# Kernel tuning notes

Measured on AMD Instinct MI355X. Metric: run time of the kernel, lower is better.

The kernel has to match this reference:

```python
import jax, jax.numpy as jnp
import numpy as np

QUERY_DIM = 192
KEY_DIM = 64
DIM_OUT = 128
C = QUERY_DIM + KEY_DIM  # 256
N = 10000
E = 320000
M = 5000


def setup_inputs() -> dict:
    key = jax.random.key(0)
    ks = jax.random.split(key, 16)
    s = 1.0 / np.sqrt(C)
    inp = {
        "query": jax.random.normal(ks[0], (N, QUERY_DIM), jnp.float32),
        "key_idx": jax.random.randint(ks[1], (N,), 0, KEY_DIM),
        "edge_index": jax.random.randint(ks[2], (2, E), 0, N),
        "mask_idx": jnp.sort(jax.random.randint(ks[3], (M,), 0, N)),
        "Wq": jax.random.normal(ks[4], (C, C), jnp.float32) * s,
        "bq": jnp.zeros((C,), jnp.float32),
        "Wk": jax.random.normal(ks[5], (C, C), jnp.float32) * s,
        "bk": jnp.zeros((C,), jnp.float32),
        "Wv": jax.random.normal(ks[6], (C, C), jnp.float32) * s,
        "bv": jnp.zeros((C,), jnp.float32),
        "Ws": jax.random.normal(ks[7], (C, C), jnp.float32) * s,
        "bs": jnp.zeros((C,), jnp.float32),
        "Wo": jax.random.normal(ks[8], (KEY_DIM, DIM_OUT), jnp.float32) * (1.0 / np.sqrt(KEY_DIM)),
        "bo": jnp.zeros((DIM_OUT,), jnp.float32),
    }
    return inp


def reference(query, key_idx, edge_index, mask_idx, Wq, bq, Wk, bk, Wv, bv, Ws, bs, Wo, bo):
    # node features: [N, C] = concat(query, one_hot(key))
    x = jnp.concatenate([query, jax.nn.one_hot(key_idx, KEY_DIM, dtype=query.dtype)], axis=1)
    src, dst = edge_index[0], edge_index[1]  # messages flow src -> dst
    # node-level projections (dense GEMMs), then edge gather
    q_n = x @ Wq + bq
    k_n = x @ Wk + bk
    v_n = x @ Wv + bv
    q = q_n[dst]  # [E, C]
    k = k_n[src]
    v = v_n[src]
    score = jnp.sum(q * k, axis=-1) / jnp.sqrt(jnp.asarray(C, x.dtype))  # [E]
    # per-destination softmax over incoming edges
    m = jax.ops.segment_max(score, dst, num_segments=N)  # [N]
    m = jnp.where(jnp.isfinite(m), m, 0.0)
    e = jnp.exp(score - m[dst])
    denom = jax.ops.segment_sum(e, dst, num_segments=N)
    alpha = e / (denom[dst] + 1e-16)
    # scatter-aggregate weighted values + root/skip connection
    agg = jax.ops.segment_sum(alpha[:, None] * v, dst, num_segments=N)  # [N, C]
    out = agg + (x @ Ws + bs)
    h = jax.nn.relu(out[mask_idx])  # [M, C]
    h = h[:, QUERY_DIM:]  # [M, KEY_DIM]
    return h @ Wo + bo  # [M, DIM_OUT]
```

## Files before the change

kernel.cpp:

```cpp
#include <hip/hip_runtime.h>

#define QDIM 192
#define KDIM 64
#define CDIM 256
#define NCOLS 640
#define DOUT 128
#define CAP 128
#define NEG_INF __int_as_float(0xFF800000)
#define LDP 200

typedef _Float16 hf2 __attribute__((ext_vector_type(2)));
typedef _Float16 half4 __attribute__((ext_vector_type(4)));
typedef _Float16 half8 __attribute__((ext_vector_type(8)));
typedef float floatx4 __attribute__((ext_vector_type(4)));

#if defined(__has_builtin)
#if __has_builtin(__builtin_amdgcn_fdot2)
#define HAVE_FDOT2 1
#endif
#endif

__device__ __forceinline__ hf2 bc_h2(unsigned u) { return __builtin_bit_cast(hf2, u); }

__device__ __forceinline__ float dot2acc(hf2 a, hf2 b, float c) {
#ifdef HAVE_FDOT2
    return __builtin_amdgcn_fdot2(a, b, c, false);
#else
    return c + (float)a[0] * (float)b[0] + (float)a[1] * (float)b[1];
#endif
}

__device__ __forceinline__ void wmap(int j, const float* Wq, const float* Wk,
                                     const float* Wv, const float* Ws,
                                     const float** W, int* wcol) {
    if (j < 256)      { *W = Wq; *wcol = j; }
    else if (j < 512) { *W = Wk; *wcol = j - 256; }
    else if (j < 576) { *W = Wv; *wcol = QDIM + (j - 512); }
    else              { *W = Ws; *wcol = QDIM + (j - 576); }
}

__global__ __launch_bounds__(256) void prep_kernel(
        const float* Wq, const float* bq, const float* Wk, const float* bk,
        const float* Wv, const float* bv, const float* Ws, const float* bs,
        _Float16* __restrict__ BhT, float* __restrict__ Ecat,
        float* __restrict__ biasc, int* __restrict__ deg, int N) {
    int t = blockIdx.x * blockDim.x + threadIdx.x;
    if (t < NCOLS * QDIM) {
        int n = t / QDIM, k = t % QDIM;
        const float* W; int wcol;
        wmap(n, Wq, Wk, Wv, Ws, &W, &wcol);
        BhT[t] = (_Float16)W[k * CDIM + wcol];
        return;
    }
    t -= NCOLS * QDIM;
    if (t < KDIM * NCOLS) {
        int c = t / NCOLS, j = t % NCOLS;
        const float* W; int wcol;
        wmap(j, Wq, Wk, Wv, Ws, &W, &wcol);
        Ecat[t] = W[(QDIM + c) * CDIM + wcol];
        return;
    }
    t -= KDIM * NCOLS;
    if (t < NCOLS) {
        const float* W; int wcol;
        const float* b;
        if (t < 256)      b = bq;
        else if (t < 512) b = bk;
        else if (t < 576) b = bv;
        else              b = bs;
        wmap(t, Wq, Wk, Wv, Ws, &W, &wcol);
        biasc[t] = b[wcol];
        return;
    }
    t -= NCOLS;
    if (t < N) deg[t] = 0;
}

__global__ __launch_bounds__(256) void gemm_nodes(
        const float* __restrict__ query, const _Float16* __restrict__ BhT,
        const int* __restrict__ key_idx, const float* __restrict__ Ecat,
        const float* __restrict__ biasc,
        _Float16* __restrict__ Qbuf, _Float16* __restrict__ Kbuf,
        float* __restrict__ Vbuf, float* __restrict__ Sbuf, int N) {
    __shared__ __align__(16) _Float16 As[64 * LDP];
    __shared__ __align__(16) _Float16 Bs[64 * LDP];
    int bm = blockIdx.x * 64;
    int bn = blockIdx.y * 64;
    int tid = threadIdx.x;

    #pragma unroll
    for (int it = 0; it < 12; it++) {
        int idx = tid + it * 256;
        int r = idx / 48, f4 = idx % 48;
        int gr = bm + r;
        float4 va = make_float4(0.f, 0.f, 0.f, 0.f);
        if (gr < N) va = ((const float4*)(query + (size_t)gr * QDIM))[f4];
        half4 h = { (_Float16)va.x, (_Float16)va.y, (_Float16)va.z, (_Float16)va.w };
        *((half4*)&As[r * LDP + f4 * 4]) = h;
    }
    #pragma unroll
    for (int it = 0; it < 6; it++) {
        int idx = tid + it * 256;
        int r = idx / 24, kg = idx % 24;
        uint4 vb = ((const uint4*)(BhT + (size_t)(bn + r) * QDIM))[kg];
        *((uint4*)&Bs[r * LDP + kg * 8]) = vb;
    }
    __syncthreads();

    int w = tid >> 6, l = tid & 63;
    int lrow = l & 15, quad = l >> 4;
    floatx4 acc[4] = {{0.f,0.f,0.f,0.f},{0.f,0.f,0.f,0.f},{0.f,0.f,0.f,0.f},{0.f,0.f,0.f,0.f}};

    const _Float16* arow = &As[(w * 16 + lrow) * LDP + quad * 8];
    #pragma unroll
    for (int ks = 0; ks < 6; ks++) {
        half8 af = *(const half8*)(arow + ks * 32);
        #pragma unroll
        for (int nt = 0; nt < 4; nt++) {
            half8 bf = *(const half8*)(&Bs[(nt * 16 + lrow) * LDP + quad * 8 + ks * 32]);
            acc[nt] = __builtin_amdgcn_mfma_f32_16x16x32_f16(af, bf, acc[nt], 0, 0, 0);
        }
    }

    int ki[4];
    #pragma unroll
    for (int reg = 0; reg < 4; reg++) {
        int gr = bm + w * 16 + quad * 4 + reg;
        ki[reg] = (gr < N) ? key_idx[gr] : 0;
    }
    #pragma unroll
    for (int nt = 0; nt < 4; nt++) {
        int gc = bn + nt * 16 + lrow;
        float bias = biasc[gc];
        #pragma unroll
        for (int reg = 0; reg < 4; reg++) {
            int gr = bm + w * 16 + quad * 4 + reg;
            if (gr < N) {
                float v = acc[nt][reg] + Ecat[ki[reg] * NCOLS + gc] + bias;
                if (gc < 256)      Qbuf[(size_t)gr * 256 + gc] = (_Float16)v;
                else if (gc < 512) Kbuf[(size_t)gr * 256 + (gc - 256)] = (_Float16)v;
                else if (gc < 576) Vbuf[(size_t)gr * KDIM + (gc - 512)] = v;
                else               Sbuf[(size_t)gr * KDIM + (gc - 576)] = v;
            }
        }
    }
}

__global__ __launch_bounds__(256) void scatter_kernel(
        const int* __restrict__ src, const int* __restrict__ dst,
        int* __restrict__ deg, int* __restrict__ adj, int E) {
    int e = blockIdx.x * blockDim.x + threadIdx.x;
    if (e < E) {
        int d = dst[e];
        int slot = atomicAdd(&deg[d], 1);
        if (slot < CAP) adj[d * CAP + slot] = src[e];
    }
}

__global__ __launch_bounds__(256) void attend_out(
        const _Float16* __restrict__ Qbuf, const _Float16* __restrict__ Kbuf,
        const float* __restrict__ Vbuf, const float* __restrict__ Sbuf,
        const int* __restrict__ deg, const int* __restrict__ adj,
        const int* __restrict__ mask, const float* __restrict__ Wo,
        const float* __restrict__ bo, float* __restrict__ out, int M) {
    int w = threadIdx.x >> 6, lane = threadIdx.x & 63;
    int r = blockIdx.x * 4 + w;
    if (r >= M) return;
    int node = mask[r];
    int l = lane & 15, g = lane >> 4;

    const uint4* qp = (const uint4*)(Qbuf + (size_t)node * 256 + l * 16);
    uint4 qa = qp[0], qb = qp[1];
    hf2 qh[8] = { bc_h2(qa.x), bc_h2(qa.y), bc_h2(qa.z), bc_h2(qa.w),
                  bc_h2(qb.x), bc_h2(qb.y), bc_h2(qb.z), bc_h2(qb.w) };

    int dn = min(deg[node], CAP);
    const int* arow = adj + (size_t)node * CAP;

    float m = NEG_INF, dsum = 0.f, accl = 0.f;
    for (int i0 = 0; i0 < dn; i0 += 4) {
        int i = i0 + g;
        int s = 0;
        float sc = NEG_INF;
        if (i < dn) {
            s = arow[i];
            const uint4* kp = (const uint4*)(Kbuf + (size_t)s * 256 + l * 16);
            uint4 ka = kp[0], kb = kp[1];
            float d = 0.f;
            d = dot2acc(bc_h2(ka.x), qh[0], d);
            d = dot2acc(bc_h2(ka.y), qh[1], d);
            d = dot2acc(bc_h2(ka.z), qh[2], d);
            d = dot2acc(bc_h2(ka.w), qh[3], d);
            d = dot2acc(bc_h2(kb.x), qh[4], d);
            d = dot2acc(bc_h2(kb.y), qh[5], d);
            d = dot2acc(bc_h2(kb.z), qh[6], d);
            d = dot2acc(bc_h2(kb.w), qh[7], d);
            d += __shfl_xor(d, 1, 64);
            d += __shfl_xor(d, 2, 64);
            d += __shfl_xor(d, 4, 64);
            d += __shfl_xor(d, 8, 64);
            sc = d * 0.0625f;
        }
        float mx = sc;
        mx = fmaxf(mx, __shfl_xor(mx, 16, 64));
        mx = fmaxf(mx, __shfl_xor(mx, 32, 64));
        float m_new = fmaxf(m, mx);
        float scale = __expf(m - m_new);
        float p = __expf(sc - m_new);
        float P = p;
        P += __shfl_xor(P, 16, 64);
        P += __shfl_xor(P, 32, 64);
        dsum = dsum * scale + P;
        m = m_new;
        float p0 = __shfl(p, 0, 64),  p1 = __shfl(p, 16, 64);
        float p2 = __shfl(p, 32, 64), p3 = __shfl(p, 48, 64);
        int   s0 = __shfl(s, 0, 64),  s1 = __shfl(s, 16, 64);
        int   s2 = __shfl(s, 32, 64), s3 = __shfl(s, 48, 64);
        float vacc = p0 * Vbuf[(size_t)s0 * KDIM + lane];
        vacc += p1 * Vbuf[(size_t)s1 * KDIM + lane];
        vacc += p2 * Vbuf[(size_t)s2 * KDIM + lane];
        vacc += p3 * Vbuf[(size_t)s3 * KDIM + lane];
        accl = accl * scale + vacc;
    }

    float h = fmaxf(accl / (dsum + 1e-16f) + Sbuf[(size_t)node * KDIM + lane], 0.f);
    float a0 = bo[lane], a1 = bo[lane + 64];
    #pragma unroll 8
    for (int c = 0; c < KDIM; c++) {
        float hv = __shfl(h, c, 64);
        a0 += hv * Wo[c * DOUT + lane];
        a1 += hv * Wo[c * DOUT + 64 + lane];
    }
    out[(size_t)r * DOUT + lane] = a0;
    out[(size_t)r * DOUT + 64 + lane] = a1;
}

extern "C" void kernel_launch(void* const* d_in, const int* in_sizes, int n_in,
                              void* d_out, int out_size, void* d_ws, size_t ws_size,
                              hipStream_t stream) {
    const float* query    = (const float*)d_in[0];
    const int* key_idx    = (const int*)d_in[1];
    const int* edge_index = (const int*)d_in[2];
    const int* mask_idx   = (const int*)d_in[3];
    const float* Wq = (const float*)d_in[4];
    const float* bq = (const float*)d_in[5];
    const float* Wk = (const float*)d_in[6];
    const float* bk = (const float*)d_in[7];
    const float* Wv = (const float*)d_in[8];
    const float* bv = (const float*)d_in[9];
    const float* Ws = (const float*)d_in[10];
    const float* bs = (const float*)d_in[11];
    const float* Wo = (const float*)d_in[12];
    const float* bo = (const float*)d_in[13];

    int N = in_sizes[0] / QDIM;
    int E = in_sizes[2] / 2;
    int M = in_sizes[3];
    const int* esrc = edge_index;
    const int* edst = edge_index + E;

    char* wsb = (char*)d_ws;
    size_t off = 0;
    auto alloc = [&](size_t nbytes) { char* p = wsb + off; off += (nbytes + 15) & ~15ull; return p; };
    _Float16* BhT  = (_Float16*)alloc((size_t)NCOLS * QDIM * 2);
    _Float16* Qbuf = (_Float16*)alloc((size_t)N * 256 * 2);
    _Float16* Kbuf = (_Float16*)alloc((size_t)N * 256 * 2);
    float* Vbuf    = (float*)alloc((size_t)N * KDIM * 4);
    float* Sbuf    = (float*)alloc((size_t)N * KDIM * 4);
    float* Ecat    = (float*)alloc((size_t)KDIM * NCOLS * 4);
    float* biasc   = (float*)alloc(NCOLS * 4);
    int*   deg     = (int*)alloc((size_t)N * 4);
    int*   adj     = (int*)alloc((size_t)N * CAP * 4);

    int prep_elems = NCOLS * QDIM + KDIM * NCOLS + NCOLS + N;
    prep_kernel<<<(prep_elems + 255) / 256, 256, 0, stream>>>(
        Wq, bq, Wk, bk, Wv, bv, Ws, bs, BhT, Ecat, biasc, deg, N);

    dim3 ggrid((N + 63) / 64, NCOLS / 64);
    gemm_nodes<<<ggrid, 256, 0, stream>>>(query, BhT, key_idx, Ecat, biasc,
                                          Qbuf, Kbuf, Vbuf, Sbuf, N);

    scatter_kernel<<<(E + 255) / 256, 256, 0, stream>>>(esrc, edst, deg, adj, E);

    attend_out<<<(M + 3) / 4, 256, 0, stream>>>(Qbuf, Kbuf, Vbuf, Sbuf, deg, adj,
                                                mask_idx, Wo, bo, (float*)d_out, M);
}
```

Baseline: 158.9 us.

## Drop prep kernel, filter edges to masked nodes, restructure attention loop

Removes the weight-prep kernel: the GEMM now reads the fp32 weights directly, converts the B tile to fp16 in shared memory, and looks up the one-hot and bias terms from the original weight arrays. Degree and marker buffers are zeroed with a memset, and the GEMM marks the masked destination nodes so the scatter only inserts edges whose destination is needed. Vbuf is stored in fp16. The attention kernel keeps a separate online softmax in each lane group and merges the groups once at the end, which removes the per-iteration shuffles. Duplicate mask rows are computed once and their output written to every matching row. In exchange the GEMM does uncoalesced strided weight loads in every block, and the fp16 V storage reduces precision.

```diff
diff --git a/kernel.cpp b/kernel.cpp
--- a/kernel.cpp
+++ b/kernel.cpp
@@ -3,7 +3,6 @@
 #define QDIM 192
 #define KDIM 64
 #define CDIM 256
-#define NCOLS 640
 #define DOUT 128
 #define CAP 128
 #define NEG_INF __int_as_float(0xFF800000)
@@ -39,54 +38,21 @@
     else              { *W = Ws; *wcol = QDIM + (j - 576); }
 }
 
-__global__ __launch_bounds__(256) void prep_kernel(
+__global__ __launch_bounds__(256) void gemm_nodes(
+        const float* __restrict__ query, const int* __restrict__ key_idx,
         const float* Wq, const float* bq, const float* Wk, const float* bk,
         const float* Wv, const float* bv, const float* Ws, const float* bs,
-        _Float16* __restrict__ BhT, float* __restrict__ Ecat,
-        float* __restrict__ biasc, int* __restrict__ deg, int N) {
-    int t = blockIdx.x * blockDim.x + threadIdx.x;
-    if (t < NCOLS * QDIM) {
-        int n = t / QDIM, k = t % QDIM;
-        const float* W; int wcol;
-        wmap(n, Wq, Wk, Wv, Ws, &W, &wcol);
-        BhT[t] = (_Float16)W[k * CDIM + wcol];
-        return;
-    }
-    t -= NCOLS * QDIM;
-    if (t < KDIM * NCOLS) {
-        int c = t / NCOLS, j = t % NCOLS;
-        const float* W; int wcol;
-        wmap(j, Wq, Wk, Wv, Ws, &W, &wcol);
-        Ecat[t] = W[(QDIM + c) * CDIM + wcol];
-        return;
-    }
-    t -= KDIM * NCOLS;
-    if (t < NCOLS) {
-        const float* W; int wcol;
-        const float* b;
-        if (t < 256)      b = bq;
-        else if (t < 512) b = bk;
-        else if (t < 576) b = bv;
-        else              b = bs;
-        wmap(t, Wq, Wk, Wv, Ws, &W, &wcol);
-        biasc[t] = b[wcol];
-        return;
-    }
-    t -= NCOLS;
-    if (t < N) deg[t] = 0;
-}
-
-__global__ __launch_bounds__(256) void gemm_nodes(
-        const float* __restrict__ query, const _Float16* __restrict__ BhT,
-        const int* __restrict__ key_idx, const float* __restrict__ Ecat,
-        const float* __restrict__ biasc,
+        const int* __restrict__ mask, int M, unsigned char* __restrict__ mrk,
         _Float16* __restrict__ Qbuf, _Float16* __restrict__ Kbuf,
-        float* __restrict__ Vbuf, float* __restrict__ Sbuf, int N) {
+        _Float16* __restrict__ Vbuf, float* __restrict__ Sbuf, int N) {
     __shared__ __align__(16) _Float16 As[64 * LDP];
     __shared__ __align__(16) _Float16 Bs[64 * LDP];
     int bm = blockIdx.x * 64;
     int bn = blockIdx.y * 64;
     int tid = threadIdx.x;
+
+    int gid = (blockIdx.y * gridDim.x + blockIdx.x) * 256 + tid;
+    if (gid < M) mrk[mask[gid]] = 1;
 
     #pragma unroll
     for (int it = 0; it < 12; it++) {
@@ -98,12 +64,14 @@
         half4 h = { (_Float16)va.x, (_Float16)va.y, (_Float16)va.z, (_Float16)va.w };
         *((half4*)&As[r * LDP + f4 * 4]) = h;
     }
-    #pragma unroll
-    for (int it = 0; it < 6; it++) {
-        int idx = tid + it * 256;
-        int r = idx / 24, kg = idx % 24;
-        uint4 vb = ((const uint4*)(BhT + (size_t)(bn + r) * QDIM))[kg];
-        *((uint4*)&Bs[r * LDP + kg * 8]) = vb;
+    {
+        int cj = tid >> 2;
+        int ks = (tid & 3) * 48;
+        const float* W; int wc;
+        wmap(bn + cj, Wq, Wk, Wv, Ws, &W, &wc);
+        #pragma unroll 8
+        for (int k = 0; k < 48; k++)
+            Bs[cj * LDP + ks + k] = (_Float16)W[(ks + k) * CDIM + wc];
     }
     __syncthreads();
 
@@ -131,15 +99,18 @@
     #pragma unroll
     for (int nt = 0; nt < 4; nt++) {
         int gc = bn + nt * 16 + lrow;
-        float bias = biasc[gc];
+        const float* W; int wc;
+        wmap(gc, Wq, Wk, Wv, Ws, &W, &wc);
+        const float* bvec = (gc < 256) ? bq : (gc < 512) ? bk : (gc < 576) ? bv : bs;
+        float bias = bvec[wc];
         #pragma unroll
         for (int reg = 0; reg < 4; reg++) {
             int gr = bm + w * 16 + quad * 4 + reg;
             if (gr < N) {
-                float v = acc[nt][reg] + Ecat[ki[reg] * NCOLS + gc] + bias;
+                float v = acc[nt][reg] + W[(QDIM + ki[reg]) * CDIM + wc] + bias;
                 if (gc < 256)      Qbuf[(size_t)gr * 256 + gc] = (_Float16)v;
                 else if (gc < 512) Kbuf[(size_t)gr * 256 + (gc - 256)] = (_Float16)v;
-                else if (gc < 576) Vbuf[(size_t)gr * KDIM + (gc - 512)] = v;
+                else if (gc < 576) Vbuf[(size_t)gr * KDIM + (gc - 512)] = (_Float16)v;
                 else               Sbuf[(size_t)gr * KDIM + (gc - 576)] = v;
             }
         }
@@ -148,18 +119,21 @@
 
 __global__ __launch_bounds__(256) void scatter_kernel(
         const int* __restrict__ src, const int* __restrict__ dst,
+        const unsigned char* __restrict__ mrk,
         int* __restrict__ deg, int* __restrict__ adj, int E) {
     int e = blockIdx.x * blockDim.x + threadIdx.x;
     if (e < E) {
         int d = dst[e];
-        int slot = atomicAdd(&deg[d], 1);
-        if (slot < CAP) adj[d * CAP + slot] = src[e];
+        if (mrk[d]) {
+            int slot = atomicAdd(&deg[d], 1);
+            if (slot < CAP) adj[d * CAP + slot] = src[e];
+        }
     }
 }
 
 __global__ __launch_bounds__(256) void attend_out(
         const _Float16* __restrict__ Qbuf, const _Float16* __restrict__ Kbuf,
-        const float* __restrict__ Vbuf, const float* __restrict__ Sbuf,
+        const _Float16* __restrict__ Vbuf, const float* __restrict__ Sbuf,
         const int* __restrict__ deg, const int* __restrict__ adj,
         const int* __restrict__ mask, const float* __restrict__ Wo,
         const float* __restrict__ bo, float* __restrict__ out, int M) {
@@ -167,6 +141,7 @@
     int r = blockIdx.x * 4 + w;
     if (r >= M) return;
     int node = mask[r];
+    if (r > 0 && mask[r - 1] == node) return;
     int l = lane & 15, g = lane >> 4;
 
     const uint4* qp = (const uint4*)(Qbuf + (size_t)node * 256 + l * 16);
@@ -177,62 +152,73 @@
     int dn = min(deg[node], CAP);
     const int* arow = adj + (size_t)node * CAP;
 
-    float m = NEG_INF, dsum = 0.f, accl = 0.f;
-    for (int i0 = 0; i0 < dn; i0 += 4) {
-        int i = i0 + g;
-        int s = 0;
-        float sc = NEG_INF;
-        if (i < dn) {
-            s = arow[i];
-            const uint4* kp = (const uint4*)(Kbuf + (size_t)s * 256 + l * 16);
-            uint4 ka = kp[0], kb = kp[1];
-            float d = 0.f;
-            d = dot2acc(bc_h2(ka.x), qh[0], d);
-            d = dot2acc(bc_h2(ka.y), qh[1], d);
-            d = dot2acc(bc_h2(ka.z), qh[2], d);
-            d = dot2acc(bc_h2(ka.w), qh[3], d);
-            d = dot2acc(bc_h2(kb.x), qh[4], d);
-            d = dot2acc(bc_h2(kb.y), qh[5], d);
-            d = dot2acc(bc_h2(kb.z), qh[6], d);
-            d = dot2acc(bc_h2(kb.w), qh[7], d);
-            d += __shfl_xor(d, 1, 64);
-            d += __shfl_xor(d, 2, 64);
-            d += __shfl_xor(d, 4, 64);
-            d += __shfl_xor(d, 8, 64);
-            sc = d * 0.0625f;
-        }
-        float mx = sc;
-        mx = fmaxf(mx, __shfl_xor(mx, 16, 64));
-        mx = fmaxf(mx, __shfl_xor(mx, 32, 64));
-        float m_new = fmaxf(m, mx);
+    float m = NEG_INF, dsum = 0.f;
+    float a0 = 0.f, a1 = 0.f, a2 = 0.f, a3 = 0.f;
+    for (int i = g; i < dn; i += 4) {
+        int s = arow[i];
+        const uint4* kp = (const uint4*)(Kbuf + (size_t)s * 256 + l * 16);
+        uint4 ka = kp[0], kb = kp[1];
+        float d = 0.f;
+        d = dot2acc(bc_h2(ka.x), qh[0], d);
+        d = dot2acc(bc_h2(ka.y), qh[1], d);
+        d = dot2acc(bc_h2(ka.z), qh[2], d);
+        d = dot2acc(bc_h2(ka.w), qh[3], d);
+        d = dot2acc(bc_h2(kb.x), qh[4], d);
+        d = dot2acc(bc_h2(kb.y), qh[5], d);
+        d = dot2acc(bc_h2(kb.z), qh[6], d);
+        d = dot2acc(bc_h2(kb.w), qh[7], d);
+        d += __shfl_xor(d, 1, 64);
+        d += __shfl_xor(d, 2, 64);
+        d += __shfl_xor(d, 4, 64);
+        d += __shfl_xor(d, 8, 64);
+        float sc = d * 0.0625f;
+        float m_new = fmaxf(m, sc);
         float scale = __expf(m - m_new);
         float p = __expf(sc - m_new);
-        float P = p;
-        P += __shfl_xor(P, 16, 64);
-        P += __shfl_xor(P, 32, 64);
-        dsum = dsum * scale + P;
+        dsum = dsum * scale + p;
+        uint2 vv = *(const uint2*)(Vbuf + (size_t)s * KDIM + l * 4);
+        hf2 v01 = bc_h2(vv.x), v23 = bc_h2(vv.y);
+        a0 = a0 * scale + p * (float)v01[0];
+        a1 = a1 * scale + p * (float)v01[1];
+        a2 = a2 * scale + p * (float)v23[0];
+        a3 = a3 * scale + p * (float)v23[1];
         m = m_new;
-        float p0 = __shfl(p, 0, 64),  p1 = __shfl(p, 16, 64);
-        float p2 = __shfl(p, 32, 64), p3 = __shfl(p, 48, 64);
-        int   s0 = __shfl(s, 0, 64),  s1 = __shfl(s, 16, 64);
-        int   s2 = __shfl(s, 32, 64), s3 = __shfl(s, 48, 64);
-        float vacc = p0 * Vbuf[(size_t)s0 * KDIM + lane];
-        vacc += p1 * Vbuf[(size_t)s1 * KDIM + lane];
-        vacc += p2 * Vbuf[(size_t)s2 * KDIM + lane];
-        vacc += p3 * Vbuf[(size_t)s3 * KDIM + lane];
-        accl = accl * scale + vacc;
-    }
-
-    float h = fmaxf(accl / (dsum + 1e-16f) + Sbuf[(size_t)node * KDIM + lane], 0.f);
-    float a0 = bo[lane], a1 = bo[lane + 64];
-    #pragma unroll 8
+    }
+
+    float Mx = fmaxf(m, __shfl_xor(m, 16, 64));
+    Mx = fmaxf(Mx, __shfl_xor(Mx, 32, 64));
+    float wgt = __expf(m - Mx);
+    if (m == NEG_INF) wgt = 0.f;
+    float ds = dsum * wgt;
+    ds += __shfl_xor(ds, 16, 64);
+    ds += __shfl_xor(ds, 32, 64);
+    a0 *= wgt; a1 *= wgt; a2 *= wgt; a3 *= wgt;
+    a0 += __shfl_xor(a0, 16, 64); a0 += __shfl_xor(a0, 32, 64);
+    a1 += __shfl_xor(a1, 16, 64); a1 += __shfl_xor(a1, 32, 64);
+    a2 += __shfl_xor(a2, 16, 64); a2 += __shfl_xor(a2, 32, 64);
+    a3 += __shfl_xor(a3, 16, 64); a3 += __shfl_xor(a3, 32, 64);
+    float inv = 1.f / (ds + 1e-16f);
+
+    float4 s4 = *((const float4*)(Sbuf + (size_t)node * KDIM + l * 4));
+    float h0 = fmaxf(a0 * inv + s4.x, 0.f);
+    float h1 = fmaxf(a1 * inv + s4.y, 0.f);
+    float h2 = fmaxf(a2 * inv + s4.z, 0.f);
+    float h3 = fmaxf(a3 * inv + s4.w, 0.f);
+
+    float o0 = bo[lane], o1 = bo[lane + 64];
+    #pragma unroll
     for (int c = 0; c < KDIM; c++) {
-        float hv = __shfl(h, c, 64);
-        a0 += hv * Wo[c * DOUT + lane];
-        a1 += hv * Wo[c * DOUT + 64 + lane];
-    }
-    out[(size_t)r * DOUT + lane] = a0;
-    out[(size_t)r * DOUT + 64 + lane] = a1;
+        float hc = (c & 3) == 0 ? h0 : (c & 3) == 1 ? h1 : (c & 3) == 2 ? h2 : h3;
+        float hv = __shfl(hc, c >> 2, 64);
+        o0 += hv * Wo[c * DOUT + lane];
+        o1 += hv * Wo[c * DOUT + 64 + lane];
+    }
+    int rr = r;
+    do {
+        out[(size_t)rr * DOUT + lane] = o0;
+        out[(size_t)rr * DOUT + 64 + lane] = o1;
+        rr++;
+    } while (rr < M && mask[rr] == node);
 }
 
 extern "C" void kernel_launch(void* const* d_in, const int* in_sizes, int n_in,
@@ -262,25 +248,22 @@
     char* wsb = (char*)d_ws;
     size_t off = 0;
     auto alloc = [&](size_t nbytes) { char* p = wsb + off; off += (nbytes + 15) & ~15ull; return p; };
-    _Float16* BhT  = (_Float16*)alloc((size_t)NCOLS * QDIM * 2);
     _Float16* Qbuf = (_Float16*)alloc((size_t)N * 256 * 2);
     _Float16* Kbuf = (_Float16*)alloc((size_t)N * 256 * 2);
-    float* Vbuf    = (float*)alloc((size_t)N * KDIM * 4);
+    _Float16* Vbuf = (_Float16*)alloc((size_t)N * KDIM * 2);
     float* Sbuf    = (float*)alloc((size_t)N * KDIM * 4);
-    float* Ecat    = (float*)alloc((size_t)KDIM * NCOLS * 4);
-    float* biasc   = (float*)alloc(NCOLS * 4);
-    int*   deg     = (int*)alloc((size_t)N * 4);
+    int*   deg     = (int*)alloc((size_t)N * 4 + (size_t)N);
+    unsigned char* mrk = (unsigned char*)(deg + N);
     int*   adj     = (int*)alloc((size_t)N * CAP * 4);
 
-    int prep_elems = NCOLS * QDIM + KDIM * NCOLS + NCOLS + N;
-    prep_kernel<<<(prep_elems + 255) / 256, 256, 0, stream>>>(
-        Wq, bq, Wk, bk, Wv, bv, Ws, bs, BhT, Ecat, biasc, deg, N);
-
-    dim3 ggrid((N + 63) / 64, NCOLS / 64);
-    gemm_nodes<<<ggrid, 256, 0, stream>>>(query, BhT, key_idx, Ecat, biasc,
+    hipMemsetAsync(deg, 0, (size_t)N * 5, stream);
+
+    dim3 ggrid((N + 63) / 64, 10);
+    gemm_nodes<<<ggrid, 256, 0, stream>>>(query, key_idx, Wq, bq, Wk, bk, Wv, bv,
+                                          Ws, bs, mask_idx, M, mrk,
                                           Qbuf, Kbuf, Vbuf, Sbuf, N);
 
-    scatter_kernel<<<(E + 255) / 256, 256, 0, stream>>>(esrc, edst, deg, adj, E);
+    scatter_kernel<<<(E + 255) / 256, 256, 0, stream>>>(esrc, edst, mrk, deg, adj, E);
 
     attend_out<<<(M + 3) / 4, 256, 0, stream>>>(Qbuf, Kbuf, Vbuf, Sbuf, deg, adj,
                                                 mask_idx, Wo, bo, (float*)d_out, M);
```

New measurement: 152.1 us. 1.04x faster.
